# Performance work log

Measured on AMD Instinct MI355X. Metric: run time of the kernel, lower is better.

The kernel has to match this reference:

```python
import jax, jax.numpy as jnp
import numpy as np

NUM_BLOCKS = 6
NUM_HEADS = 8
DIM = 49
SCALE = float(np.sqrt(DIM) + 1e-6)  # sqrt(49)+eps as in the torch code


def setup_inputs() -> dict:
    key = jax.random.key(0)
    ks = jax.random.split(key, 16)
    B, P = 64, 512
    s = 0.1  # keep activations well-scaled
    return {
        "embedding": jax.random.normal(ks[0], (B, P, DIM), jnp.float32),
        "target_labels": jax.random.randint(ks[1], (B,), 0, 10),
        "Wq": jax.random.normal(ks[2], (NUM_BLOCKS, NUM_HEADS, DIM, DIM), jnp.float32) * s,
        "bq": jax.random.normal(ks[3], (NUM_BLOCKS, NUM_HEADS, DIM), jnp.float32) * s,
        "Wk": jax.random.normal(ks[4], (NUM_BLOCKS, NUM_HEADS, DIM, DIM), jnp.float32) * s,
        "bk": jax.random.normal(ks[5], (NUM_BLOCKS, NUM_HEADS, DIM), jnp.float32) * s,
        "Wv": jax.random.normal(ks[6], (NUM_BLOCKS, NUM_HEADS, DIM, DIM), jnp.float32) * s,
        "bv": jax.random.normal(ks[7], (NUM_BLOCKS, NUM_HEADS, DIM), jnp.float32) * s,
        "Wh": jax.random.normal(ks[8], (NUM_BLOCKS, NUM_HEADS, DIM, DIM), jnp.float32) * s,
        "bh": jax.random.normal(ks[9], (NUM_BLOCKS, NUM_HEADS, DIM), jnp.float32) * s,
        "Wout": jax.random.normal(ks[10], (NUM_BLOCKS, DIM, NUM_HEADS * DIM), jnp.float32) * s,
        "W1": jax.random.normal(ks[11], (25, DIM), jnp.float32) * s,
        "b1": jax.random.normal(ks[12], (25,), jnp.float32) * s,
        "W2": jax.random.normal(ks[13], (10, 25), jnp.float32) * s,
        "b2": jax.random.normal(ks[14], (10,), jnp.float32) * s,
    }


def reference(embedding, target_labels, Wq, bq, Wk, bk, Wv, bv, Wh, bh, Wout, W1, b1, W2, b2):
    B, P, D = embedding.shape
    x = embedding
    for l in range(NUM_BLOCKS):  # fixed small structural loop over blocks
        # per-head projections, all heads batched: [B,H,P,D]
        Q = jnp.einsum('bpi,hoi->bhpo', x, Wq[l]) + bq[l][:, None, :]
        K = jnp.einsum('bpi,hoi->bhpo', x, Wk[l]) + bk[l][:, None, :]
        V = jnp.einsum('bpi,hoi->bhpo', x, Wv[l]) + bv[l][:, None, :]
        scores = jnp.einsum('bhpo,bhqo->bhpq', Q, K) / SCALE
        scores = jnp.clip(scores, -30.0, 30.0)
        weights = jax.nn.softmax(scores, axis=-1)
        attn_out = jnp.einsum('bhpq,bhqo->bhpo', weights, V)
        head_out = jnp.einsum('bhpo,hdo->bhpd', attn_out, Wh[l]) + bh[l][:, None, :]
        # concat head outputs along feature dim (head order preserved): [B,P,H*D]
        concat = head_out.transpose(0, 2, 1, 3).reshape(B, P, NUM_HEADS * D)
        # out-projection uses weight only (no bias), as in the torch forward
        x = jnp.einsum('bpc,oc->bpo', concat, Wout[l])
    pooled = x.mean(axis=1)  # [B, D]
    h = jax.nn.relu(pooled @ W1.T + b1)
    logits = h @ W2.T + b2  # [B, 10]
    logp = jax.nn.log_softmax(logits, axis=-1)
    loss = -jnp.take_along_axis(logp, target_labels[:, None], axis=1).mean()
    return loss
```

## Files before the change

kernel.cpp:

```cpp
#include <hip/hip_runtime.h>
#include <hip/hip_bf16.h>
#include <math.h>

#define Bn 64
#define Pn 512
#define Hn 8
#define Ln 6

typedef __bf16 bf16x8 __attribute__((ext_vector_type(8)));
typedef float f32x4 __attribute__((ext_vector_type(4)));

#define VMCNT(n) asm volatile("s_waitcnt vmcnt(" #n ")" ::: "memory")
#define LGKM0()  asm volatile("s_waitcnt lgkmcnt(0)" ::: "memory")

static __device__ __forceinline__ unsigned short f2bf(float f) {
    return __builtin_bit_cast(unsigned short, __float2bfloat16(f));
}
static __device__ __forceinline__ float bf2f(unsigned short v) {
    unsigned int u = ((unsigned int)v) << 16;
    return __builtin_bit_cast(float, u);
}
static __device__ __forceinline__ float fexp2(float x) {
    float r;
    asm("v_exp_f32 %0, %1" : "=v"(r) : "v"(x));
    return r;
}
static __device__ __forceinline__ unsigned cvtpk(float a, float b) {
    unsigned r;
    asm("v_cvt_pk_bf16_f32 %0, %1, %2" : "=v"(r) : "v"(a), "v"(b));
    return r;
}

#define C1F (1.4426950408889634f / 7.000001f)
#define C2F 43.2808512f

__global__ __launch_bounds__(256)
void prep_wqkv_kernel(const float* __restrict__ Wq, const float* __restrict__ Wk,
                      const float* __restrict__ Wv, unsigned short* __restrict__ out) {
    int idx = blockIdx.x * 256 + threadIdx.x;
    if (idx >= Ln * 3 * Hn * 4096) return;
    int i = idx & 63, o = (idx >> 6) & 63, h = (idx >> 12) & 7, t = idx >> 15;
    int mat = t % 3, l = t / 3;
    float v = 0.f;
    if (o < 49 && i < 49) {
        const float* src = (mat == 0) ? Wq : (mat == 1) ? Wk : Wv;
        v = src[(((size_t)(l * Hn + h) * 49) + o) * 49 + i];
    }
    out[idx] = f2bf(v);
}

__global__ __launch_bounds__(256)
void prep_weff_kernel(const float* __restrict__ Wh, const float* __restrict__ bh,
                      const float* __restrict__ Wout,
                      unsigned short* __restrict__ Weff, float* __restrict__ beff) {
    const int NW = Ln * Hn * 4096;
    int idx = blockIdx.x * 256 + threadIdx.x;
    if (idx < NW) {
        int o = idx & 63, o2 = (idx >> 6) & 63, h = (idx >> 12) & 7, l = idx >> 15;
        float s = 0.f;
        if (o < 49 && o2 < 49) {
            const float* wh = Wh + ((size_t)(l * Hn + h) * 49) * 49 + o;
            const float* wo = Wout + ((size_t)l * 49 + o2) * 392 + h * 49;
            for (int dd = 0; dd < 49; ++dd) s = fmaf(wh[dd * 49], wo[dd], s);
        }
        Weff[idx] = f2bf(s);
    } else if (idx < NW + Ln * 49) {
        int j = idx - NW;
        int l = j / 49, o2 = j % 49;
        const float* wo = Wout + ((size_t)l * 49 + o2) * 392;
        const float* bhl = bh + (size_t)l * 392;
        float s = 0.f;
        for (int cc = 0; cc < 392; ++cc) s = fmaf(bhl[cc], wo[cc], s);
        beff[j] = s;
    }
}

__global__ __launch_bounds__(256)
void cast_x_kernel(const float* __restrict__ emb, unsigned short* __restrict__ xbf) {
    int idx = blockIdx.x * 256 + threadIdx.x;
    int row = idx >> 6, col = idx & 63;
    float v = (col < 49) ? emb[(size_t)row * 49 + col] : 0.f;
    xbf[idx] = f2bf(v);
}

__global__ __launch_bounds__(256)
void qkv_mfma_kernel(const unsigned short* __restrict__ xbf,
                     const unsigned short* __restrict__ Wqkv,
                     const float* __restrict__ bq_l, const float* __restrict__ bk_l,
                     const float* __restrict__ bv_l,
                     unsigned short* __restrict__ Qb, unsigned short* __restrict__ Kb,
                     unsigned short* __restrict__ Vt,
                     int b_off, int Bc) {
    __shared__ uint4 xlb4[512];
    __shared__ uint4 wlb4[512];
    __shared__ __align__(16) unsigned short stg[64 * 68];
    __shared__ __align__(16) float blds[1536];
    char* xlb = (char*)xlb4;
    char* wlb = (char*)wlb4;
    const int tid = threadIdx.x;
    const int w = tid >> 6, lane = tid & 63, g = lane >> 4, c = lane & 15;
    const int flat = blockIdx.x;
    const int bl = flat % Bc;
    const int tile = flat / Bc;
    const int r0 = bl * Pn + tile * 64;

    for (int t = tid; t < 1536; t += 256) {
        int mat = t >> 9, rem = t & 511, h = rem >> 6, o = rem & 63;
        const float* bb = (mat == 0) ? bq_l : (mat == 1) ? bk_l : bv_l;
        blds[t] = (o < 49) ? bb[h * 49 + o] : 0.f;
    }
    {
        const unsigned short* xg = xbf + ((size_t)b_off * Pn + r0) * 64;
        #pragma unroll
        for (int i = 0; i < 2; ++i) {
            int chunk = tid + i * 256;
            int row = chunk >> 3, c8 = chunk & 7;
            *(uint4*)(xlb + row * 128 + 16 * (c8 ^ (row & 7))) =
                *(const uint4*)(xg + row * 64 + c8 * 8);
        }
    }
    __syncthreads();

    const int rowa = w * 16 + c;
    bf16x8 a0 = *(const bf16x8*)(xlb + rowa * 128 + 16 * ((g    ) ^ (c & 7)));
    bf16x8 a1 = *(const bf16x8*)(xlb + rowa * 128 + 16 * ((g + 4) ^ (c & 7)));

    for (int panel = 0; panel < 24; ++panel) {
        const int mat = panel >> 3, h = panel & 7;
        const unsigned short* wg = Wqkv + (size_t)panel * 4096;
        #pragma unroll
        for (int i = 0; i < 2; ++i) {
            int chunk = tid + i * 256;
            int row = chunk >> 3, c8 = chunk & 7;
            *(uint4*)(wlb + row * 128 + 16 * (c8 ^ (row & 7))) =
                *(const uint4*)(wg + row * 64 + c8 * 8);
        }
        __syncthreads();

        f32x4 acc[4];
        #pragma unroll
        for (int bt = 0; bt < 4; ++bt) acc[bt] = (f32x4){0.f, 0.f, 0.f, 0.f};
        const float* bbB = blds + mat * 512 + h * 64;

        if (mat < 2) {
            #pragma unroll
            for (int bt = 0; bt < 4; ++bt) {
                int rowb = bt * 16 + c;
                bf16x8 w0 = *(const bf16x8*)(wlb + rowb * 128 + 16 * ((g    ) ^ (rowb & 7)));
                bf16x8 w1 = *(const bf16x8*)(wlb + rowb * 128 + 16 * ((g + 4) ^ (rowb & 7)));
                acc[bt] = __builtin_amdgcn_mfma_f32_16x16x32_bf16(w0, a0, acc[bt], 0, 0, 0);
                acc[bt] = __builtin_amdgcn_mfma_f32_16x16x32_bf16(w1, a1, acc[bt], 0, 0, 0);
            }
            const int p = w * 16 + c;
            #pragma unroll
            for (int bt = 0; bt < 4; ++bt) {
                f32x4 bb4 = *(const f32x4*)(bbB + bt * 16 + 4 * g);
                float v0 = acc[bt][0] + bb4[0];
                float v1 = acc[bt][1] + bb4[1];
                float v2 = acc[bt][2] + bb4[2];
                float v3 = acc[bt][3] + bb4[3];
                if (mat == 0) { v0 *= C1F; v1 *= C1F; v2 *= C1F; v3 *= C1F; }
                if (bt == 3) {
                    float q49 = (mat == 0) ? -C2F : 1.0f;
                    bool g0 = (g == 0);
                    v0 = g0 ? v0 : 0.f;
                    v1 = g0 ? q49 : 0.f;
                    v2 = 0.f; v3 = 0.f;
                }
                uint2 pk = {cvtpk(v0, v1), cvtpk(v2, v3)};
                *(uint2*)((char*)stg + p * 136 + (bt * 16 + 4 * g) * 2) = pk;
            }
        } else {
            #pragma unroll
            for (int bt = 0; bt < 4; ++bt) {
                int rowb = bt * 16 + c;
                bf16x8 w0 = *(const bf16x8*)(wlb + rowb * 128 + 16 * ((g    ) ^ (rowb & 7)));
                bf16x8 w1 = *(const bf16x8*)(wlb + rowb * 128 + 16 * ((g + 4) ^ (rowb & 7)));
                acc[bt] = __builtin_amdgcn_mfma_f32_16x16x32_bf16(a0, w0, acc[bt], 0, 0, 0);
                acc[bt] = __builtin_amdgcn_mfma_f32_16x16x32_bf16(a1, w1, acc[bt], 0, 0, 0);
            }
            #pragma unroll
            for (int bt = 0; bt < 4; ++bt) {
                int d = bt * 16 + c;
                float bbd = bbB[d];
                float v0 = acc[bt][0] + bbd;
                float v1 = acc[bt][1] + bbd;
                float v2 = acc[bt][2] + bbd;
                float v3 = acc[bt][3] + bbd;
                if (bt == 3) {
                    bool is49 = (c == 1);
                    v0 = is49 ? 1.0f : v0;
                    v1 = is49 ? 1.0f : v1;
                    v2 = is49 ? 1.0f : v2;
                    v3 = is49 ? 1.0f : v3;
                }
                uint2 pk = {cvtpk(v0, v1), cvtpk(v2, v3)};
                *(uint2*)((char*)stg + d * 136 + (w * 16 + 4 * g) * 2) = pk;
            }
        }
        __syncthreads();

        if (mat < 2) {
            unsigned short* outp = (mat == 0) ? Qb : Kb;
            #pragma unroll
            for (int i = 0; i < 4; ++i) {
                int chunk = tid + i * 256;
                int prow = chunk >> 4, c4 = chunk & 15;
                uint2 v = *(const uint2*)((const char*)stg + prow * 136 + c4 * 8);
                int rr = r0 + prow;
                int bl2 = rr >> 9, p = rr & 511;
                *(uint2*)(outp + (((size_t)bl2 * Hn + h) * Pn + p) * 64 + c4 * 4) = v;
            }
        } else {
            const int bl2 = r0 >> 9, p0 = r0 & 511;
            #pragma unroll
            for (int i = 0; i < 4; ++i) {
                int chunk = tid + i * 256;
                int drow = chunk >> 4, c4 = chunk & 15;
                uint2 v = *(const uint2*)((const char*)stg + drow * 136 + c4 * 8);
                *(uint2*)(Vt + (((size_t)bl2 * Hn + h) * 64 + drow) * Pn + p0 + c4 * 4) = v;
            }
        }
        __syncthreads();
    }
}

__global__ __launch_bounds__(256, 4)
void attn_head_kernel(const unsigned short* __restrict__ Qb,
                      const unsigned short* __restrict__ Kb,
                      const unsigned short* __restrict__ Vt,
                      unsigned short* __restrict__ AO,
                      int Bc) {
    __shared__ uint4 lds4[2048];
    char* ldsb = (char*)lds4;
    const int tid = threadIdx.x;
    const int w = tid >> 6, lane = tid & 63, g = lane >> 4, c = lane & 15;
    const int flat = blockIdx.x;
    const int x = flat & 7;
    const int qt = (flat >> 3) & 3;
    const int a = flat >> 5;
    const size_t bh = (size_t)(a * 8 + x);
    const int q0 = qt * 128;

    bf16x8 qf[2][2];
    #pragma unroll
    for (int qs = 0; qs < 2; ++qs) {
        const unsigned short* qp = Qb + (bh * Pn + q0 + w * 32 + qs * 16 + c) * 64;
        qf[qs][0] = *(const bf16x8*)(qp + g * 8);
        qf[qs][1] = *(const bf16x8*)(qp + g * 8 + 32);
    }
    f32x4 oacc[2][4];
    #pragma unroll
    for (int qs = 0; qs < 2; ++qs)
        #pragma unroll
        for (int dt = 0; dt < 4; ++dt)
            oacc[qs][dt] = (f32x4){0.f, 0.f, 0.f, 0.f};

    const unsigned short* Kg0 = Kb + bh * (size_t)(Pn * 64);
    const unsigned short* Vg0 = Vt + bh * (size_t)(64 * Pn);

    auto stage = [&](int kt, int buf) {
        const unsigned short* Kg = Kg0 + kt * (64 * 64);
        const unsigned short* Vg = Vg0 + kt * 64;
        #pragma unroll
        for (int j = 0; j < 2; ++j) {
            int chunk = w * 128 + j * 64 + lane;
            int row = chunk >> 3, c8 = chunk & 7;
            int swc = (c8 ^ (row & 7)) << 3;
            __builtin_amdgcn_global_load_lds(
                (const __attribute__((address_space(1))) void*)(Kg + row * 64 + swc),
                (__attribute__((address_space(3))) void*)(ldsb + buf * 8192 + w * 2048 + j * 1024),
                16, 0, 0);
            __builtin_amdgcn_global_load_lds(
                (const __attribute__((address_space(1))) void*)(Vg + (size_t)row * Pn + swc),
                (__attribute__((address_space(3))) void*)(ldsb + 16384 + buf * 8192 + w * 2048 + j * 1024),
                16, 0, 0);
        }
    };

    stage(0, 0);

    #pragma unroll 2
    for (int kt = 0; kt < 8; ++kt) {
        const int cur = kt & 1;
        VMCNT(0);
        __builtin_amdgcn_s_barrier();
        __builtin_amdgcn_sched_barrier(0);
        if (kt < 7) stage(kt + 1, cur ^ 1);
        __builtin_amdgcn_sched_barrier(0);

        char* Klb = ldsb + cur * 8192;
        char* Vlb = ldsb + 16384 + cur * 8192;

        unsigned up01[2][4], up23[2][4];
        #pragma unroll
        for (int t = 0; t < 4; ++t) {
            const int krow = t * 16 + c;
            bf16x8 kf0 = *(const bf16x8*)(Klb + krow * 128 + 16 * ((g    ) ^ (krow & 7)));
            bf16x8 kf1 = *(const bf16x8*)(Klb + krow * 128 + 16 * ((g + 4) ^ (krow & 7)));
            #pragma unroll
            for (int qs = 0; qs < 2; ++qs) {
                f32x4 s4 = {0.f, 0.f, 0.f, 0.f};
                __builtin_amdgcn_s_setprio(1);
                s4 = __builtin_amdgcn_mfma_f32_16x16x32_bf16(kf0, qf[qs][0], s4, 0, 0, 0);
                s4 = __builtin_amdgcn_mfma_f32_16x16x32_bf16(kf1, qf[qs][1], s4, 0, 0, 0);
                __builtin_amdgcn_s_setprio(0);
                float p0 = fexp2(s4[0]);
                float p1 = fexp2(s4[1]);
                float p2 = fexp2(s4[2]);
                float p3 = fexp2(s4[3]);
                up01[qs][t] = cvtpk(p0, p1);
                up23[qs][t] = cvtpk(p2, p3);
            }
        }

        #pragma unroll
        for (int kk = 0; kk < 2; ++kk) {
            bf16x8 pa[2];
            #pragma unroll
            for (int qs = 0; qs < 2; ++qs) {
                unsigned d0 = up01[qs][2 * kk], d2 = up01[qs][2 * kk + 1];
                unsigned d1 = up23[qs][2 * kk], d3 = up23[qs][2 * kk + 1];
                asm("v_permlane32_swap_b32 %0, %1" : "+v"(d0), "+v"(d2));
                asm("v_permlane16_swap_b32 %0, %1" : "+v"(d0), "+v"(d2));
                asm("v_permlane32_swap_b32 %0, %1" : "+v"(d1), "+v"(d3));
                asm("v_permlane16_swap_b32 %0, %1" : "+v"(d1), "+v"(d3));
                uint4 uv = {d0, d1, d2, d3};
                pa[qs] = __builtin_bit_cast(bf16x8, uv);
            }
            __builtin_amdgcn_s_setprio(1);
            #pragma unroll
            for (int dt = 0; dt < 4; ++dt) {
                const int vrow = dt * 16 + c;
                bf16x8 vf = *(const bf16x8*)(Vlb + vrow * 128 + 16 * ((g + 4 * kk) ^ (vrow & 7)));
                oacc[0][dt] = __builtin_amdgcn_mfma_f32_16x16x32_bf16(pa[0], vf, oacc[0][dt], 0, 0, 0);
                oacc[1][dt] = __builtin_amdgcn_mfma_f32_16x16x32_bf16(pa[1], vf, oacc[1][dt], 0, 0, 0);
            }
            __builtin_amdgcn_s_setprio(0);
        }
    }
    __builtin_amdgcn_s_barrier();

    float rinv[2][4];
    #pragma unroll
    for (int qs = 0; qs < 2; ++qs)
        #pragma unroll
        for (int r = 0; r < 4; ++r) {
            float s = __shfl(oacc[qs][3][r], (lane & 48) | 1);
            rinv[qs][r] = 1.0f / s;
        }
    char* stgw = ldsb + w * 4096;
    #pragma unroll
    for (int qs = 0; qs < 2; ++qs)
        #pragma unroll
        for (int dt = 0; dt < 4; ++dt)
            #pragma unroll
            for (int r = 0; r < 4; ++r) {
                int prow = qs * 16 + 4 * g + r;
                int col = dt * 16 + c;
                *(unsigned short*)(stgw + prow * 128 + ((2 * col) ^ ((prow & 7) << 4))) =
                    f2bf(oacc[qs][dt][r] * rinv[qs][r]);
            }
    LGKM0();
    __builtin_amdgcn_sched_barrier(0);
    #pragma unroll
    for (int i = 0; i < 4; ++i) {
        int chunk = i * 64 + lane;
        int row = chunk >> 3, c8 = chunk & 7;
        uint4 v = *(const uint4*)(stgw + row * 128 + 16 * (c8 ^ (row & 7)));
        size_t grow = bh * Pn + q0 + w * 32 + row;
        *(uint4*)(AO + grow * 64 + c8 * 8) = v;
    }
}

__global__ __launch_bounds__(256)
void outqkv_kernel(const unsigned short* __restrict__ AO,
                   const unsigned short* __restrict__ Weffl,
                   const float* __restrict__ beffl,
                   const unsigned short* __restrict__ Wqkv,
                   const float* __restrict__ bq_l, const float* __restrict__ bk_l,
                   const float* __restrict__ bv_l,
                   unsigned short* __restrict__ Qb, unsigned short* __restrict__ Kb,
                   unsigned short* __restrict__ Vt,
                   unsigned short* __restrict__ xout,
                   int last, int b_off, int Bc) {
    __shared__ uint4 lds4[2592];
    __shared__ __align__(16) float blds[1536];
    __shared__ __align__(16) float bldc[64];
    char* ldsb = (char*)lds4;
    unsigned short* stg = (unsigned short*)(ldsb + 32768);
    const int tid = threadIdx.x;
    const int w = tid >> 6, lane = tid & 63, g = lane >> 4, c = lane & 15;
    const int flat = blockIdx.x;
    const int bl = flat % Bc;
    const int tile = flat / Bc;
    const int p0 = tile * 64;
    const int r0 = bl * Pn + p0;

    if (!last) {
        for (int t = tid; t < 1536; t += 256) {
            int mat = t >> 9, rem = t & 511, h = rem >> 6, o = rem & 63;
            const float* bb = (mat == 0) ? bq_l : (mat == 1) ? bk_l : bv_l;
            blds[t] = (o < 49) ? bb[h * 49 + o] : 0.f;
        }
    }
    if (tid < 64) bldc[tid] = (tid < 49) ? beffl[tid] : 0.f;

    const int chunk0 = w * 128 + lane;
    const int rowL0 = chunk0 >> 3, c8L0 = chunk0 & 7;
    const int swc0 = (c8L0 ^ (rowL0 & 7)) << 3;
    const int chunk1 = chunk0 + 64;
    const int rowL1 = chunk1 >> 3, c8L1 = chunk1 & 7;
    const int swc1 = (c8L1 ^ (rowL1 & 7)) << 3;

    auto stageW = [&](const unsigned short* Wg, int buf) {
        __builtin_amdgcn_global_load_lds(
            (const __attribute__((address_space(1))) void*)(Wg + rowL0 * 64 + swc0),
            (__attribute__((address_space(3))) void*)(ldsb + 16384 + buf * 8192 + w * 2048),
            16, 0, 0);
        __builtin_amdgcn_global_load_lds(
            (const __attribute__((address_space(1))) void*)(Wg + rowL1 * 64 + swc1),
            (__attribute__((address_space(3))) void*)(ldsb + 16384 + buf * 8192 + w * 2048 + 1024),
            16, 0, 0);
    };
    auto stageA = [&](const unsigned short* Ag, int buf) {
        __builtin_amdgcn_global_load_lds(
            (const __attribute__((address_space(1))) void*)(Ag + rowL0 * 64 + swc0),
            (__attribute__((address_space(3))) void*)(ldsb + buf * 8192 + w * 2048),
            16, 0, 0);
        __builtin_amdgcn_global_load_lds(
            (const __attribute__((address_space(1))) void*)(Ag + rowL1 * 64 + swc1),
            (__attribute__((address_space(3))) void*)(ldsb + buf * 8192 + w * 2048 + 1024),
            16, 0, 0);
    };

    f32x4 acc[4];
    #pragma unroll
    for (int bt = 0; bt < 4; ++bt) acc[bt] = (f32x4){0.f, 0.f, 0.f, 0.f};

    stageA(AO + (((size_t)bl * Hn + 0) * Pn + p0) * 64, 0);
    stageW(Weffl, 0);
    for (int h = 0; h < Hn; ++h) {
        const int cur = h & 1;
        VMCNT(0);
        __builtin_amdgcn_s_barrier();
        __builtin_amdgcn_sched_barrier(0);
        if (h < 7) {
            stageA(AO + (((size_t)bl * Hn + h + 1) * Pn + p0) * 64, cur ^ 1);
            stageW(Weffl + (size_t)(h + 1) * 4096, cur ^ 1);
        }
        __builtin_amdgcn_sched_barrier(0);
        char* Alb = ldsb + cur * 8192;
        char* Wlb = ldsb + 16384 + cur * 8192;
        const int rowa = w * 16 + c;
        bf16x8 a0 = *(const bf16x8*)(Alb + rowa * 128 + 16 * ((g    ) ^ (c & 7)));
        bf16x8 a1 = *(const bf16x8*)(Alb + rowa * 128 + 16 * ((g + 4) ^ (c & 7)));
        #pragma unroll
        for (int bt = 0; bt < 4; ++bt) {
            int rowb = bt * 16 + c;
            bf16x8 w0 = *(const bf16x8*)(Wlb + rowb * 128 + 16 * ((g    ) ^ (rowb & 7)));
            bf16x8 w1 = *(const bf16x8*)(Wlb + rowb * 128 + 16 * ((g + 4) ^ (rowb & 7)));
            acc[bt] = __builtin_amdgcn_mfma_f32_16x16x32_bf16(w0, a0, acc[bt], 0, 0, 0);
            acc[bt] = __builtin_amdgcn_mfma_f32_16x16x32_bf16(w1, a1, acc[bt], 0, 0, 0);
        }
    }

    const int p = w * 16 + c;
    if (last) {
        __syncthreads();
        #pragma unroll
        for (int bt = 0; bt < 4; ++bt) {
            f32x4 bb4 = *(const f32x4*)(bldc + bt * 16 + 4 * g);
            uint2 pk = {cvtpk(acc[bt][0] + bb4[0], acc[bt][1] + bb4[1]),
                        cvtpk(acc[bt][2] + bb4[2], acc[bt][3] + bb4[3])};
            *(uint2*)((char*)stg + p * 136 + (bt * 16 + 4 * g) * 2) = pk;
        }
        LGKM0();
        __syncthreads();
        #pragma unroll
        for (int i = 0; i < 4; ++i) {
            int chunk = tid + i * 256;
            int prow = chunk >> 4, c4 = chunk & 15;
            uint2 v = *(const uint2*)((const char*)stg + prow * 136 + c4 * 8);
            size_t grow = (size_t)(b_off + bl) * Pn + p0 + prow;
            *(uint2*)(xout + grow * 64 + c4 * 4) = v;
        }
        return;
    }

    #pragma unroll
    for (int bt = 0; bt < 4; ++bt) {
        f32x4 bb4 = *(const f32x4*)(bldc + bt * 16 + 4 * g);
        uint2 pk = {cvtpk(acc[bt][0] + bb4[0], acc[bt][1] + bb4[1]),
                    cvtpk(acc[bt][2] + bb4[2], acc[bt][3] + bb4[3])};
        *(uint2*)(ldsb + p * 128 + ((2 * (bt * 16 + 4 * g)) ^ ((p & 7) << 4))) = pk;
    }
    stageW(Wqkv, 0);

    VMCNT(0);
    LGKM0();
    __builtin_amdgcn_s_barrier();
    __builtin_amdgcn_sched_barrier(0);

    const int rowa = w * 16 + c;
    bf16x8 a0 = *(const bf16x8*)(ldsb + rowa * 128 + 16 * ((g    ) ^ (c & 7)));
    bf16x8 a1 = *(const bf16x8*)(ldsb + rowa * 128 + 16 * ((g + 4) ^ (c & 7)));

    for (int panel = 0; panel < 24; ++panel) {
        const int mat = panel >> 3, h = panel & 7;
        const int cur = panel & 1;
        if (panel > 0) {
            VMCNT(0);
            __builtin_amdgcn_s_barrier();
            __builtin_amdgcn_sched_barrier(0);
        }
        if (panel < 23) stageW(Wqkv + (size_t)(panel + 1) * 4096, cur ^ 1);
        __builtin_amdgcn_sched_barrier(0);
        char* Wlb = ldsb + 16384 + cur * 8192;

        f32x4 pacc[4];
        #pragma unroll
        for (int bt = 0; bt < 4; ++bt) pacc[bt] = (f32x4){0.f, 0.f, 0.f, 0.f};
        const float* bbB = blds + mat * 512 + h * 64;

        if (mat < 2) {
            #pragma unroll
            for (int bt = 0; bt < 4; ++bt) {
                int rowb = bt * 16 + c;
                bf16x8 w0 = *(const bf16x8*)(Wlb + rowb * 128 + 16 * ((g    ) ^ (rowb & 7)));
                bf16x8 w1 = *(const bf16x8*)(Wlb + rowb * 128 + 16 * ((g + 4) ^ (rowb & 7)));
                pacc[bt] = __builtin_amdgcn_mfma_f32_16x16x32_bf16(w0, a0, pacc[bt], 0, 0, 0);
                pacc[bt] = __builtin_amdgcn_mfma_f32_16x16x32_bf16(w1, a1, pacc[bt], 0, 0, 0);
            }
            #pragma unroll
            for (int bt = 0; bt < 4; ++bt) {
                f32x4 bb4 = *(const f32x4*)(bbB + bt * 16 + 4 * g);
                float v0 = pacc[bt][0] + bb4[0];
                float v1 = pacc[bt][1] + bb4[1];
                float v2 = pacc[bt][2] + bb4[2];
                float v3 = pacc[bt][3] + bb4[3];
                if (mat == 0) { v0 *= C1F; v1 *= C1F; v2 *= C1F; v3 *= C1F; }
                if (bt == 3) {
                    float q49 = (mat == 0) ? -C2F : 1.0f;
                    bool g0 = (g == 0);
                    v0 = g0 ? v0 : 0.f;
                    v1 = g0 ? q49 : 0.f;
                    v2 = 0.f; v3 = 0.f;
                }
                uint2 pk = {cvtpk(v0, v1), cvtpk(v2, v3)};
                *(uint2*)((char*)stg + p * 136 + (bt * 16 + 4 * g) * 2) = pk;
            }
        } else {
            #pragma unroll
            for (int bt = 0; bt < 4; ++bt) {
                int rowb = bt * 16 + c;
                bf16x8 w0 = *(const bf16x8*)(Wlb + rowb * 128 + 16 * ((g    ) ^ (rowb & 7)));
                bf16x8 w1 = *(const bf16x8*)(Wlb + rowb * 128 + 16 * ((g + 4) ^ (rowb & 7)));
                pacc[bt] = __builtin_amdgcn_mfma_f32_16x16x32_bf16(a0, w0, pacc[bt], 0, 0, 0);
                pacc[bt] = __builtin_amdgcn_mfma_f32_16x16x32_bf16(a1, w1, pacc[bt], 0, 0, 0);
            }
            #pragma unroll
            for (int bt = 0; bt < 4; ++bt) {
                int d = bt * 16 + c;
                float bbd = bbB[d];
                float v0 = pacc[bt][0] + bbd;
                float v1 = pacc[bt][1] + bbd;
                float v2 = pacc[bt][2] + bbd;
                float v3 = pacc[bt][3] + bbd;
                if (bt == 3) {
                    bool is49 = (c == 1);
                    v0 = is49 ? 1.0f : v0;
                    v1 = is49 ? 1.0f : v1;
                    v2 = is49 ? 1.0f : v2;
                    v3 = is49 ? 1.0f : v3;
                }
                uint2 pk = {cvtpk(v0, v1), cvtpk(v2, v3)};
                *(uint2*)((char*)stg + d * 136 + (w * 16 + 4 * g) * 2) = pk;
            }
        }
        LGKM0();
        __builtin_amdgcn_s_barrier();

        if (mat < 2) {
            unsigned short* outp = (mat == 0) ? Qb : Kb;
            #pragma unroll
            for (int i = 0; i < 4; ++i) {
                int chunk = tid + i * 256;
                int prow = chunk >> 4, c4 = chunk & 15;
                uint2 v = *(const uint2*)((const char*)stg + prow * 136 + c4 * 8);
                int rr = r0 + prow;
                int bl2 = rr >> 9, pp = rr & 511;
                *(uint2*)(outp + (((size_t)bl2 * Hn + h) * Pn + pp) * 64 + c4 * 4) = v;
            }
        } else {
            #pragma unroll
            for (int i = 0; i < 4; ++i) {
                int chunk = tid + i * 256;
                int drow = chunk >> 4, c4 = chunk & 15;
                uint2 v = *(const uint2*)((const char*)stg + drow * 136 + c4 * 8);
                *(uint2*)(Vt + (((size_t)bl * Hn + h) * 64 + drow) * Pn + p0 + c4 * 4) = v;
            }
        }
    }
}

__global__ __launch_bounds__(256)
void pool_kernel(const unsigned short* __restrict__ x, float* __restrict__ pooled) {
    __shared__ float red[256];
    const int b = blockIdx.x;
    const int tid = threadIdx.x;
    const int ps = tid >> 6, d = tid & 63;
    float s = 0.f;
    for (int p = ps; p < Pn; p += 4) s += bf2f(x[((size_t)b * Pn + p) * 64 + d]);
    red[tid] = s;
    __syncthreads();
    if (tid < 64) {
        float t = red[tid] + red[tid + 64] + red[tid + 128] + red[tid + 192];
        if (tid < 49) pooled[b * 49 + tid] = t * (1.0f / Pn);
    }
}

__global__ __launch_bounds__(64)
void head_kernel(const float* __restrict__ pooled, const int* __restrict__ labels,
                 const float* __restrict__ W1, const float* __restrict__ b1,
                 const float* __restrict__ W2, const float* __restrict__ b2,
                 float* __restrict__ out) {
    __shared__ float lloss[64];
    const int b = threadIdx.x;
    float pr[49];
    #pragma unroll
    for (int i = 0; i < 49; ++i) pr[i] = pooled[b * 49 + i];
    float hh[25];
    for (int j = 0; j < 25; ++j) {
        float s = b1[j];
        for (int i = 0; i < 49; ++i) s = fmaf(pr[i], W1[j * 49 + i], s);
        hh[j] = fmaxf(s, 0.f);
    }
    float lg[10];
    float m = -1e30f;
    for (int k = 0; k < 10; ++k) {
        float s = b2[k];
        for (int j = 0; j < 25; ++j) s = fmaf(hh[j], W2[k * 25 + j], s);
        lg[k] = s;
        m = fmaxf(m, s);
    }
    float se = 0.f;
    for (int k = 0; k < 10; ++k) se += __expf(lg[k] - m);
    float lse = m + __logf(se);
    int lbl = labels[b];
    lloss[b] = lse - lg[lbl];
    __syncthreads();
    if (b == 0) {
        float s = 0.f;
        for (int i = 0; i < 64; ++i) s += lloss[i];
        out[0] = s * (1.0f / 64.0f);
    }
}

extern "C" void kernel_launch(void* const* d_in, const int* in_sizes, int n_in,
                              void* d_out, int out_size, void* d_ws, size_t ws_size,
                              hipStream_t stream) {
    const float* emb    = (const float*)d_in[0];
    const int*   labels = (const int*)d_in[1];
    const float* Wq = (const float*)d_in[2];
    const float* bq = (const float*)d_in[3];
    const float* Wk = (const float*)d_in[4];
    const float* bk = (const float*)d_in[5];
    const float* Wv = (const float*)d_in[6];
    const float* bv = (const float*)d_in[7];
    const float* Wh = (const float*)d_in[8];
    const float* bhp = (const float*)d_in[9];
    const float* Wout = (const float*)d_in[10];
    const float* W1 = (const float*)d_in[11];
    const float* b1 = (const float*)d_in[12];
    const float* W2 = (const float*)d_in[13];
    const float* b2 = (const float*)d_in[14];
    float* out = (float*)d_out;

    char* base = (char*)d_ws;
    size_t off = 0;
    auto alloc = [&](size_t bytes) {
        off = (off + 255) & ~(size_t)255;
        char* p = base + off;
        off += bytes;
        return p;
    };

    unsigned short* WqkvB = (unsigned short*)alloc((size_t)Ln * 3 * Hn * 4096 * 2);
    unsigned short* WeffB = (unsigned short*)alloc((size_t)Ln * Hn * 4096 * 2);
    float*          beffB = (float*)alloc((size_t)Ln * 49 * 4);
    unsigned short* xA    = (unsigned short*)alloc((size_t)Bn * Pn * 64 * 2);
    unsigned short* xB    = (unsigned short*)alloc((size_t)Bn * Pn * 64 * 2);
    float*          pooled = (float*)alloc((size_t)Bn * 49 * 4);

    const size_t per_b = 4 * ((size_t)Hn * Pn * 64 * 2);
    size_t fixed = (off + 255) & ~(size_t)255;
    int Bc = Bn;
    while (Bc > 8 && fixed + (size_t)Bc * per_b + 4096 > ws_size) Bc >>= 1;

    unsigned short* Qb  = (unsigned short*)alloc((size_t)Bc * Hn * Pn * 64 * 2);
    unsigned short* Kb  = (unsigned short*)alloc((size_t)Bc * Hn * Pn * 64 * 2);
    unsigned short* Vtb = (unsigned short*)alloc((size_t)Bc * Hn * Pn * 64 * 2);
    unsigned short* AOb = (unsigned short*)alloc((size_t)Bc * Hn * Pn * 64 * 2);

    prep_wqkv_kernel<<<(Ln * 3 * Hn * 4096 + 255) / 256, 256, 0, stream>>>(Wq, Wk, Wv, WqkvB);
    prep_weff_kernel<<<(Ln * Hn * 4096 + Ln * 49 + 255) / 256, 256, 0, stream>>>(Wh, bhp, Wout, WeffB, beffB);
    cast_x_kernel<<<(Bn * Pn * 64) / 256, 256, 0, stream>>>(emb, xA);

    for (int b0 = 0; b0 < Bn; b0 += Bc) {
        qkv_mfma_kernel<<<Bc * 8, 256, 0, stream>>>(
            xA, WqkvB, bq, bk, bv, Qb, Kb, Vtb, b0, Bc);
        for (int l = 0; l < Ln; ++l) {
            attn_head_kernel<<<Bc * 32, 256, 0, stream>>>(Qb, Kb, Vtb, AOb, Bc);
            int last = (l == Ln - 1) ? 1 : 0;
            int ln = last ? 0 : (l + 1);
            outqkv_kernel<<<Bc * 8, 256, 0, stream>>>(
                AOb,
                WeffB + (size_t)l * Hn * 4096,
                beffB + (size_t)l * 49,
                WqkvB + (size_t)ln * 3 * Hn * 4096,
                bq + (size_t)ln * Hn * 49,
                bk + (size_t)ln * Hn * 49,
                bv + (size_t)ln * Hn * 49,
                Qb, Kb, Vtb, xB, last, b0, Bc);
        }
    }

    pool_kernel<<<Bn, 256, 0, stream>>>(xB, pooled);
    head_kernel<<<1, 64, 0, stream>>>(pooled, labels, W1, b1, W2, b2, out);
}
```

Before: 504.4 us.

## Widen attention blocks to 512 threads and triple-buffer outqkv loads

The attention kernel now uses 512-thread blocks that each cover 256 queries, so every staged K/V tile is shared by eight waves instead of four, and the grid is halved. The out-projection/QKV kernel moves from double to triple buffering: it prefetches two stages ahead and waits on partial vmcnt counts instead of draining all loads each step. The aim is to halve K/V reloads per head and hide global-load latency behind the MFMA work. In exchange the blocks get larger and outqkv uses more LDS, which may lower occupancy, and the `__launch_bounds__(512, 8)` hint puts pressure on registers.

```diff
diff --git a/kernel.cpp b/kernel.cpp
--- a/kernel.cpp
+++ b/kernel.cpp
@@ -225,7 +225,7 @@
     }
 }
 
-__global__ __launch_bounds__(256, 4)
+__global__ __launch_bounds__(512, 8)
 void attn_head_kernel(const unsigned short* __restrict__ Qb,
                       const unsigned short* __restrict__ Kb,
                       const unsigned short* __restrict__ Vt,
@@ -237,10 +237,10 @@
     const int w = tid >> 6, lane = tid & 63, g = lane >> 4, c = lane & 15;
     const int flat = blockIdx.x;
     const int x = flat & 7;
-    const int qt = (flat >> 3) & 3;
-    const int a = flat >> 5;
+    const int qt = (flat >> 3) & 1;
+    const int a = flat >> 4;
     const size_t bh = (size_t)(a * 8 + x);
-    const int q0 = qt * 128;
+    const int q0 = qt * 256;
 
     bf16x8 qf[2][2];
     #pragma unroll
@@ -259,23 +259,19 @@
     const unsigned short* Kg0 = Kb + bh * (size_t)(Pn * 64);
     const unsigned short* Vg0 = Vt + bh * (size_t)(64 * Pn);
 
+    const int rowS = tid >> 3, c8S = tid & 7;
+    const int swcS = (c8S ^ (rowS & 7)) << 3;
     auto stage = [&](int kt, int buf) {
         const unsigned short* Kg = Kg0 + kt * (64 * 64);
         const unsigned short* Vg = Vg0 + kt * 64;
-        #pragma unroll
-        for (int j = 0; j < 2; ++j) {
-            int chunk = w * 128 + j * 64 + lane;
-            int row = chunk >> 3, c8 = chunk & 7;
-            int swc = (c8 ^ (row & 7)) << 3;
-            __builtin_amdgcn_global_load_lds(
-                (const __attribute__((address_space(1))) void*)(Kg + row * 64 + swc),
-                (__attribute__((address_space(3))) void*)(ldsb + buf * 8192 + w * 2048 + j * 1024),
-                16, 0, 0);
-            __builtin_amdgcn_global_load_lds(
-                (const __attribute__((address_space(1))) void*)(Vg + (size_t)row * Pn + swc),
-                (__attribute__((address_space(3))) void*)(ldsb + 16384 + buf * 8192 + w * 2048 + j * 1024),
-                16, 0, 0);
-        }
+        __builtin_amdgcn_global_load_lds(
+            (const __attribute__((address_space(1))) void*)(Kg + rowS * 64 + swcS),
+            (__attribute__((address_space(3))) void*)(ldsb + buf * 8192 + w * 1024),
+            16, 0, 0);
+        __builtin_amdgcn_global_load_lds(
+            (const __attribute__((address_space(1))) void*)(Vg + (size_t)rowS * Pn + swcS),
+            (__attribute__((address_space(3))) void*)(ldsb + 16384 + buf * 8192 + w * 1024),
+            16, 0, 0);
     };
 
     stage(0, 0);
@@ -384,11 +380,11 @@
                    unsigned short* __restrict__ Vt,
                    unsigned short* __restrict__ xout,
                    int last, int b_off, int Bc) {
-    __shared__ uint4 lds4[2592];
+    __shared__ uint4 lds4[3616];
     __shared__ __align__(16) float blds[1536];
     __shared__ __align__(16) float bldc[64];
     char* ldsb = (char*)lds4;
-    unsigned short* stg = (unsigned short*)(ldsb + 32768);
+    unsigned short* stg = (unsigned short*)(ldsb + 49152);
     const int tid = threadIdx.x;
     const int w = tid >> 6, lane = tid & 63, g = lane >> 4, c = lane & 15;
     const int flat = blockIdx.x;
@@ -416,11 +412,11 @@
     auto stageW = [&](const unsigned short* Wg, int buf) {
         __builtin_amdgcn_global_load_lds(
             (const __attribute__((address_space(1))) void*)(Wg + rowL0 * 64 + swc0),
-            (__attribute__((address_space(3))) void*)(ldsb + 16384 + buf * 8192 + w * 2048),
+            (__attribute__((address_space(3))) void*)(ldsb + 24576 + buf * 8192 + w * 2048),
             16, 0, 0);
         __builtin_amdgcn_global_load_lds(
             (const __attribute__((address_space(1))) void*)(Wg + rowL1 * 64 + swc1),
-            (__attribute__((address_space(3))) void*)(ldsb + 16384 + buf * 8192 + w * 2048 + 1024),
+            (__attribute__((address_space(3))) void*)(ldsb + 24576 + buf * 8192 + w * 2048 + 1024),
             16, 0, 0);
     };
     auto stageA = [&](const unsigned short* Ag, int buf) {
@@ -440,18 +436,20 @@
 
     stageA(AO + (((size_t)bl * Hn + 0) * Pn + p0) * 64, 0);
     stageW(Weffl, 0);
+    stageA(AO + (((size_t)bl * Hn + 1) * Pn + p0) * 64, 1);
+    stageW(Weffl + 4096, 1);
     for (int h = 0; h < Hn; ++h) {
-        const int cur = h & 1;
-        VMCNT(0);
+        const int cur = h % 3;
+        if (h < 7) { VMCNT(4); } else { VMCNT(0); }
         __builtin_amdgcn_s_barrier();
         __builtin_amdgcn_sched_barrier(0);
-        if (h < 7) {
-            stageA(AO + (((size_t)bl * Hn + h + 1) * Pn + p0) * 64, cur ^ 1);
-            stageW(Weffl + (size_t)(h + 1) * 4096, cur ^ 1);
+        if (h < 6) {
+            stageA(AO + (((size_t)bl * Hn + h + 2) * Pn + p0) * 64, (h + 2) % 3);
+            stageW(Weffl + (size_t)(h + 2) * 4096, (h + 2) % 3);
         }
         __builtin_amdgcn_sched_barrier(0);
         char* Alb = ldsb + cur * 8192;
-        char* Wlb = ldsb + 16384 + cur * 8192;
+        char* Wlb = ldsb + 24576 + cur * 8192;
         const int rowa = w * 16 + c;
         bf16x8 a0 = *(const bf16x8*)(Alb + rowa * 128 + 16 * ((g    ) ^ (c & 7)));
         bf16x8 a1 = *(const bf16x8*)(Alb + rowa * 128 + 16 * ((g + 4) ^ (c & 7)));
@@ -496,11 +494,10 @@
         *(uint2*)(ldsb + p * 128 + ((2 * (bt * 16 + 4 * g)) ^ ((p & 7) << 4))) = pk;
     }
     stageW(Wqkv, 0);
-
-    VMCNT(0);
     LGKM0();
     __builtin_amdgcn_s_barrier();
     __builtin_amdgcn_sched_barrier(0);
+    stageW(Wqkv + 4096, 1);
 
     const int rowa = w * 16 + c;
     bf16x8 a0 = *(const bf16x8*)(ldsb + rowa * 128 + 16 * ((g    ) ^ (c & 7)));
@@ -508,15 +505,13 @@
 
     for (int panel = 0; panel < 24; ++panel) {
         const int mat = panel >> 3, h = panel & 7;
-        const int cur = panel & 1;
-        if (panel > 0) {
-            VMCNT(0);
-            __builtin_amdgcn_s_barrier();
-            __builtin_amdgcn_sched_barrier(0);
-        }
-        if (panel < 23) stageW(Wqkv + (size_t)(panel + 1) * 4096, cur ^ 1);
+        const int cur = panel % 3;
+        if (panel < 23) { VMCNT(2); } else { VMCNT(0); }
+        __builtin_amdgcn_s_barrier();
         __builtin_amdgcn_sched_barrier(0);
-        char* Wlb = ldsb + 16384 + cur * 8192;
+        if (panel < 22) stageW(Wqkv + (size_t)(panel + 2) * 4096, (panel + 2) % 3);
+        __builtin_amdgcn_sched_barrier(0);
+        char* Wlb = ldsb + 24576 + cur * 8192;
 
         f32x4 pacc[4];
         #pragma unroll
@@ -711,7 +706,7 @@
         qkv_mfma_kernel<<<Bc * 8, 256, 0, stream>>>(
             xA, WqkvB, bq, bk, bv, Qb, Kb, Vtb, b0, Bc);
         for (int l = 0; l < Ln; ++l) {
-            attn_head_kernel<<<Bc * 32, 256, 0, stream>>>(Qb, Kb, Vtb, AOb, Bc);
+            attn_head_kernel<<<Bc * 16, 512, 0, stream>>>(Qb, Kb, Vtb, AOb, Bc);
             int last = (l == Ln - 1) ? 1 : 0;
             int ln = last ? 0 : (l + 1);
             outqkv_kernel<<<Bc * 8, 256, 0, stream>>>(
```

Measured after the change: 1.046 ms. +107.4%, slower.
